# Kernel tuning notes

Measured on AMD Instinct MI355X. Metric: run time of the kernel, lower is better.

Reference implementation:

```python
import jax, jax.numpy as jnp
import numpy as np
import math
from jax import lax

RNN = 256
N_MELS = 80
RF = 5
FRAME = N_MELS * RF  # 400
DYN_CH = 8
DYN_K = 21
STATIC_CH = 8
STATIC_K = 21
PRIOR_LEN = 11


def _betabinom_pmf(n, a, b):
    k = np.arange(n + 1, dtype=np.float64)
    lg = lambda x: np.array([math.lgamma(float(v)) for v in np.atleast_1d(x)])
    logC = lg(n + 1) - lg(k + 1) - lg(n - k + 1)
    logB = lg(k + a) + lg(n - k + b) - lg(np.full_like(k, n + a + b))
    logB0 = math.lgamma(a) + math.lgamma(b) - math.lgamma(a + b)
    return np.exp(logC + logB - logB0)

# prior buffer, flipped as in the torch module (register_buffer('P', ...flip(0)))
PRIOR = jnp.asarray(_betabinom_pmf(PRIOR_LEN - 1, 0.1, 0.9)[::-1].copy(), dtype=jnp.float32)


def gru_cell(x, h, wi, bi, wh, bh):
    # torch GRUCell math
    gi = x @ wi.T + bi
    gh = h @ wh.T + bh
    ir, iz, i_n = jnp.split(gi, 3, axis=-1)
    hr, hz, h_n = jnp.split(gh, 3, axis=-1)
    r = jax.nn.sigmoid(ir + hr)
    z = jax.nn.sigmoid(iz + hz)
    n = jnp.tanh(i_n + r * h_n)
    return (1.0 - z) * n + z * h


def dca(s, alpha, dW_w, dW_b, dV_w, dF_w, dU_w, dT_w, dT_b, dv_w):
    B, S = alpha.shape
    # betabinomial prior: causal conv with flipped pmf
    ap = jnp.pad(alpha, ((0, 0), (PRIOR_LEN - 1, 0)))[:, None, :]  # [B,1,S+10]
    p = lax.conv_general_dilated(ap, PRIOR.reshape(1, 1, -1), (1,), [(0, 0)],
                                 dimension_numbers=('NCH', 'OIH', 'NCH'))[:, 0]  # [B,S]
    p = jnp.log(jnp.clip(p, 1e-6))
    # dynamic filters: one set of 8 kernels per batch element
    G = jnp.tanh(s @ dW_w.T + dW_b) @ dV_w.T  # [B, 8*21]
    g = lax.conv_general_dilated(alpha[None, :, :], G.reshape(B * DYN_CH, 1, DYN_K),
                                 (1,), [((DYN_K - 1) // 2,) * 2],
                                 dimension_numbers=('NCH', 'OIH', 'NCH'),
                                 feature_group_count=B)  # [1, B*8, S]
    g = g.reshape(B, DYN_CH, S).transpose(0, 2, 1)  # [B,S,8]
    # static filters
    f = lax.conv_general_dilated(alpha[:, None, :], dF_w, (1,), [((STATIC_K - 1) // 2,) * 2],
                                 dimension_numbers=('NCH', 'OIH', 'NCH')).transpose(0, 2, 1)  # [B,S,8]
    e = (jnp.tanh(f @ dU_w.T + g @ dT_w.T + dT_b) @ dv_w.T)[..., 0] + p  # [B,S]
    return jax.nn.softmax(e, axis=-1)


def _decode(encoder_outputs, p1_w, p1_b, p2_w, p2_b, a_wi, a_bi, a_wh, a_bh,
            dW_w, dW_b, dV_w, dF_w, dU_w, dT_w, dT_b, dv_w, l_w, l_b,
            g1_wi, g1_bi, g1_wh, g1_bh, g2_wi, g2_bi, g2_wh, g2_bh, pr_w, pr_b, T_dec):
    B, S, _ = encoder_outputs.shape
    frame0 = jnp.zeros((B, FRAME), jnp.float32)
    alpha0 = jnp.zeros((B, S), jnp.float32).at[:, 0].set(1.0)
    ctx0 = jnp.zeros((B, 3 * RNN), jnp.float32)
    h0 = jnp.zeros((B, RNN), jnp.float32)

    def step(carry, _):
        frame, alpha, ctx, h_att, h1, h2 = carry
        # pre-net (eval mode: dropout is identity)
        pre = jax.nn.relu(jax.nn.relu(frame @ p1_w.T + p1_b) @ p2_w.T + p2_b)  # [B,128]
        h_att = gru_cell(jnp.concatenate([ctx, pre], axis=-1), h_att, a_wi, a_bi, a_wh, a_bh)
        alpha = dca(h_att, alpha, dW_w, dW_b, dV_w, dF_w, dU_w, dT_w, dT_b, dv_w)
        ctx = jnp.einsum('bs,bsd->bd', alpha, encoder_outputs)  # [B,768]
        x = jnp.concatenate([ctx, h_att], axis=-1) @ l_w.T + l_b  # [B,256]
        h1 = gru_cell(x, h1, g1_wi, g1_bi, g1_wh, g1_bh)
        x = x + h1
        h2 = gru_cell(x, h2, g2_wi, g2_bi, g2_wh, g2_bh)
        x = x + h2
        out = x @ pr_w.T + pr_b  # [B,400]
        return (out, alpha, ctx, h_att, h1, h2), out

    (_, alphaT, _, _, _, _), outs = lax.scan(step, (frame0, alpha0, ctx0, h0, h0, h0), None, length=T_dec)
    # outs: [T,B,400] -> [B,80,T*5]
    mel = outs.reshape(T_dec, B, N_MELS, RF).transpose(1, 2, 0, 3).reshape(B, N_MELS, T_dec * RF)
    return mel


def setup_inputs() -> dict:
    key = jax.random.key(0)
    ks = iter(jax.random.split(key, 40))
    w = lambda shape: jax.random.normal(next(ks), shape, jnp.float32) * 0.05
    z = lambda shape: jnp.zeros(shape, jnp.float32)
    B, S, D = 64, 512, 768
    return {
        'encoder_outputs': jax.random.normal(next(ks), (B, S, D), jnp.float32),
        'p1_w': w((RNN, FRAME)), 'p1_b': z((RNN,)),
        'p2_w': w((RNN // 2, RNN)), 'p2_b': z((RNN // 2,)),
        'a_wi': w((3 * RNN, 896)), 'a_bi': z((3 * RNN,)), 'a_wh': w((3 * RNN, RNN)), 'a_bh': z((3 * RNN,)),
        'dW_w': w((128, RNN)), 'dW_b': z((128,)),
        'dV_w': w((DYN_CH * DYN_K, 128)),
        'dF_w': w((STATIC_CH, 1, STATIC_K)),
        'dU_w': w((128, STATIC_CH)),
        'dT_w': w((128, DYN_CH)), 'dT_b': z((128,)),
        'dv_w': w((1, 128)),
        'l_w': w((RNN, 4 * RNN)), 'l_b': z((RNN,)),
        'g1_wi': w((3 * RNN, RNN)), 'g1_bi': z((3 * RNN,)), 'g1_wh': w((3 * RNN, RNN)), 'g1_bh': z((3 * RNN,)),
        'g2_wi': w((3 * RNN, RNN)), 'g2_bi': z((3 * RNN,)), 'g2_wh': w((3 * RNN, RNN)), 'g2_bh': z((3 * RNN,)),
        'pr_w': w((FRAME, RNN)), 'pr_b': z((FRAME,)),
        'T_dec': 250,
    }


def reference(encoder_outputs, p1_w, p1_b, p2_w, p2_b, a_wi, a_bi, a_wh, a_bh,
              dW_w, dW_b, dV_w, dF_w, dU_w, dT_w, dT_b, dv_w, l_w, l_b,
              g1_wi, g1_bi, g1_wh, g1_bh, g2_wi, g2_bi, g2_wh, g2_bh, pr_w, pr_b, T_dec):
    return _decode(encoder_outputs, p1_w, p1_b, p2_w, p2_b, a_wi, a_bi, a_wh, a_bh,
                   dW_w, dW_b, dV_w, dF_w, dU_w, dT_w, dT_b, dv_w, l_w, l_b,
                   g1_wi, g1_bi, g1_wh, g1_bh, g2_wi, g2_bi, g2_wh, g2_bh, pr_w, pr_b, T_dec)
```

## Files before the change

### kernel.cpp

```cpp
#include <hip/hip_runtime.h>
#include <cmath>

#define TDEC 250
#define EPS_A 1e-6f

#define NB_GIC  64
#define NB_GA   128
#define NB_WH1  144
#define NB_WH2  152
#define NBLK    160

#define B_CTX(p)  (8192   + (p)*49152)
#define B_HATT(p) (106496 + (p)*16384)
#define B_H1(p)   (139264 + (p)*16384)
#define B_H2(p)   (172032 + (p)*16384)
#define B_GIC(p)  (204800 + (p)*49152)
#define B_GH(p)   (303104 + (p)*49152)
#define B_GH1(p)  (401408 + (p)*49152)
#define B_GH2(p)  (499712 + (p)*49152)
#define ZERO_END  598016
#define CVT_OFF   598016

#define OP1    0u
#define OP2    106496u
#define OAWIP  139264u
#define ODW    237568u
#define ODV    270336u
#define OLW    291840u
#define OG1I   553984u
#define OG2I   750592u
#define OPR    947200u
#define OAWI   1049600u
#define OAWH   1737728u
#define OG1H   1934336u
#define OG2H   2130944u

struct Prior { float v[11]; };

struct KArgs {
  const float *enc;
  const float *p1w,*p1b,*p2w,*p2b;
  const float *awi,*abi,*awh,*abh;
  const float *dWw,*dWb,*dVw,*dFw,*dUw,*dTw,*dTb,*dvw;
  const float *lw,*lb;
  const float *g1wi,*g1bi,*g1wh,*g1bh;
  const float *g2wi,*g2bi,*g2wh,*g2bh;
  const float *prw,*prb;
  float* ws; float* dout;
  Prior pr;
};

__device__ __forceinline__ float gld(const float* p) {
  return __uint_as_float(__hip_atomic_load((const unsigned*)p, __ATOMIC_RELAXED, __HIP_MEMORY_SCOPE_AGENT));
}
__device__ __forceinline__ void gst(float* p, float v) {
  __hip_atomic_store((unsigned*)p, __float_as_uint(v), __ATOMIC_RELAXED, __HIP_MEMORY_SCOPE_AGENT);
}
__device__ __forceinline__ float sigm(float x) { return 1.f / (1.f + expf(-x)); }

__device__ __forceinline__ float dot8(uint4 w, float4 x0, float4 x1) {
  float a;
  a = __uint_as_float(w.x << 16) * x0.x;
  a = fmaf(__uint_as_float(w.x & 0xffff0000u), x0.y, a);
  a = fmaf(__uint_as_float(w.y << 16),         x0.z, a);
  a = fmaf(__uint_as_float(w.y & 0xffff0000u), x0.w, a);
  a = fmaf(__uint_as_float(w.z << 16),         x1.x, a);
  a = fmaf(__uint_as_float(w.z & 0xffff0000u), x1.y, a);
  a = fmaf(__uint_as_float(w.w << 16),         x1.z, a);
  a = fmaf(__uint_as_float(w.w & 0xffff0000u), x1.w, a);
  return a;
}

__global__ __launch_bounds__(256) void k_init(float* ws) {
  int idx = blockIdx.x * 256 + threadIdx.x;
  for (int i = idx; i < ZERO_END; i += gridDim.x * 256) ws[i] = 0.f;
}

struct CvtSeg { const float* src; unsigned dst; unsigned N, K, KP, sstr, soff, mode; };
struct CvtArgs { CvtSeg s[13]; };
__global__ __launch_bounds__(256) void k_cvt(CvtArgs c, unsigned short* wb) {
  for (int seg = 0; seg < 13; ++seg) {
    CvtSeg sg = c.s[seg];
    unsigned short* d = wb + sg.dst;
    unsigned tot = sg.N * sg.KP;
    for (unsigned i = blockIdx.x * 256 + threadIdx.x; i < tot; i += gridDim.x * 256) {
      if (sg.mode == 0) {
        unsigned u = __float_as_uint(sg.src[i]);
        d[i] = (unsigned short)((u + 0x7fffu + ((u >> 16) & 1u)) >> 16);
      } else {
        unsigned n = i / sg.KP, k = i - n * sg.KP;
        unsigned short v = 0;
        if (k < sg.K) {
          unsigned u = __float_as_uint(sg.src[(size_t)n * sg.sstr + sg.soff + k]);
          v = (unsigned short)((u + 0x7fffu + ((u >> 16) & 1u)) >> 16);
        }
        d[(k >> 3) * (sg.N * 8) + n * 8 + (k & 7)] = v;
      }
    }
  }
}

__device__ __forceinline__ void postw(unsigned* fl, int word, unsigned v) {
  asm volatile("s_waitcnt vmcnt(0)" ::: "memory");
  __syncthreads();
  if (threadIdx.x == 0)
    __hip_atomic_store(&fl[blockIdx.x * 32 + word], v, __ATOMIC_RELAXED, __HIP_MEMORY_SCOPE_AGENT);
}
template <int SLP>
__device__ __forceinline__ void pollge(unsigned* fl, int line, int word, unsigned v) {
  while (__hip_atomic_load(&fl[line * 32 + word], __ATOMIC_RELAXED, __HIP_MEMORY_SCOPE_AGENT) < v)
    __builtin_amdgcn_s_sleep(SLP);
}

__global__ __launch_bounds__(1024, 1) void k_decode(KArgs A) {
  __shared__ __align__(16) float sm[16640];
  float* ws = A.ws;
  unsigned* fl = (unsigned*)ws;
  const unsigned short* wb = (const unsigned short*)(ws + CVT_OFF);
  const int blk = blockIdx.x;
  const int tid = threadIdx.x;

  if (blk < 64) {
    const int b = blk, bg = b >> 4;
    float* alpha = sm;
    float* hattl = sm + 512;
    float* h1l   = sm + 768;
    float* h2l   = sm + 1024;
    float* fr    = sm + 1280;
    float* xcat  = sm + 1696;
    float* xl    = sm + 2728;
    float* x2l   = sm + 2984;
    float* x3l   = sm + 3240;
    float* sal   = sm + 3496;
    float* h1s   = sm + 4040;
    float* pre   = sm + 4296;
    float* sgi   = sm + 4424;
    float* sgh   = sm + 5192;
    float* t1    = sm + 5960;
    float* Gl    = sm + 6088;
    float* sdF   = sm + 6264;
    float* sdU   = sm + 6440;
    float* sdT   = sm + 7464;
    float* sdtb  = sm + 8488;
    float* sdv   = sm + 8616;
    float* es    = sm + 8744;
    float* e     = sm + 9768;
    float* red   = sm + 10280;
    int*   wc    = (int*)(sm + 10296);
    float* lv    = sm + 10304;
    short* li    = (short*)(sm + 10816);
    float* pt    = sm + 11072;

    if (tid < 512) alpha[tid] = (tid == 0) ? 1.f : 0.f;
    if (tid < 256) { hattl[tid] = 0.f; h1l[tid] = 0.f; h2l[tid] = 0.f; xcat[768 + tid] = 0.f; }
    if (tid < 416) fr[tid] = 0.f;
    if (tid < 176) sdF[tid] = (tid < 168) ? A.dFw[tid] : 0.f;
    sdU[tid] = A.dUw[tid];
    sdT[tid] = A.dTw[tid];
    if (tid < 128) { sdtb[tid] = A.dTb[tid]; sdv[tid] = A.dvw[tid]; }
    __syncthreads();

    for (int t = 0; t < TDEC; ++t) {
      const int p = t & 1;
      if (tid < 544) { int sg = tid - 10; sal[tid] = (sg >= 0 && sg < 512) ? alpha[sg] : 0.f; }
      __syncthreads();
      {
        int part = tid >> 8, j = tid & 255;
        const float4* xr = (const float4*)fr;
        float a = 0.f;
#pragma unroll
        for (int g = 0; g < 13; ++g) {
          int gg = part * 13 + g;
          uint4 w = *(const uint4*)(wb + OP1 + (size_t)gg * 2048 + j * 8);
          a += dot8(w, xr[gg * 2], xr[gg * 2 + 1]);
        }
        pt[part * 260 + j] = a;
      }
      __syncthreads();
      if (tid < 256) h1s[tid] = fmaxf(pt[tid] + pt[260 + tid] + pt[520 + tid] + pt[780 + tid] + A.p1b[tid], 0.f);
      __syncthreads();
      {
        int part = tid >> 7, j = tid & 127;
        const float4* xr = (const float4*)h1s;
        float a = 0.f;
#pragma unroll
        for (int g = 0; g < 4; ++g) {
          int gg = part * 4 + g;
          uint4 w = *(const uint4*)(wb + OP2 + (size_t)gg * 1024 + j * 8);
          a += dot8(w, xr[gg * 2], xr[gg * 2 + 1]);
        }
        pt[part * 132 + j] = a;
      }
      __syncthreads();
      if (tid < 128) {
        float a = A.p2b[tid];
#pragma unroll
        for (int q = 0; q < 8; ++q) a += pt[q * 132 + tid];
        pre[tid] = fmaxf(a, 0.f);
      }
      __syncthreads();
      float gipre = 0.f;
      if (tid < 768) {
        const float4* xr = (const float4*)pre;
        float a = 0.f;
#pragma unroll
        for (int g = 0; g < 16; ++g) {
          uint4 w = *(const uint4*)(wb + OAWIP + (size_t)g * 6144 + tid * 8);
          a += dot8(w, xr[g * 2], xr[g * 2 + 1]);
        }
        gipre = a;
      } else if (tid < 784) {
        pollge<1>(fl, NB_GIC + bg * 16 + (tid - 768), 0, (unsigned)(t + 1));
      } else if (tid < 788) {
        pollge<1>(fl, NB_GA + bg * 4 + (tid - 784), 0, (unsigned)(t + 1));
      }
      __syncthreads();
      if (tid < 768) {
        sgi[tid] = gipre + gld(ws + B_GIC(p) + b * 768 + tid) + A.abi[tid];
        sgh[tid] = gld(ws + B_GH(p) + b * 768 + tid) + A.abh[tid];
      }
      __syncthreads();
      if (tid < 256) {
        float r = sigm(sgi[tid] + sgh[tid]);
        float z = sigm(sgi[256 + tid] + sgh[256 + tid]);
        float n = tanhf(sgi[512 + tid] + r * sgh[512 + tid]);
        float hnew = (1.f - z) * n + z * hattl[tid];
        hattl[tid] = hnew;
        xcat[768 + tid] = hnew;
        gst(ws + B_HATT(p) + b * 256 + tid, hnew);
      }
      postw(fl, 1, (unsigned)(t + 1));
      {
        int part = tid >> 7, j = tid & 127;
        const float4* xr = (const float4*)hattl;
        float a = 0.f;
#pragma unroll
        for (int g = 0; g < 4; ++g) {
          int gg = part * 4 + g;
          uint4 w = *(const uint4*)(wb + ODW + (size_t)gg * 1024 + j * 8);
          a += dot8(w, xr[gg * 2], xr[gg * 2 + 1]);
        }
        pt[part * 132 + j] = a;
      }
      __syncthreads();
      if (tid < 128) {
        float a = A.dWb[tid];
#pragma unroll
        for (int q = 0; q < 8; ++q) a += pt[q * 132 + tid];
        t1[tid] = tanhf(a);
      }
      __syncthreads();
      if (tid < 672) {
        int part = tid / 168, j = tid - part * 168;
        const float4* xr = (const float4*)t1;
        float a = 0.f;
#pragma unroll
        for (int g = 0; g < 4; ++g) {
          int gg = part * 4 + g;
          uint4 w = *(const uint4*)(wb + ODV + (size_t)gg * 1344 + j * 8);
          a += dot8(w, xr[gg * 2], xr[gg * 2 + 1]);
        }
        pt[part * 172 + j] = a;
      }
      __syncthreads();
      if (tid < 168) Gl[tid] = pt[tid] + pt[172 + tid] + pt[344 + tid] + pt[516 + tid];
      __syncthreads();
      {
        int sl = tid >> 1, half = tid & 1;
        float f0[8], g0[8];
#pragma unroll
        for (int q = 0; q < 8; ++q) {
          float fa = 0.f, ga = 0.f;
#pragma unroll
          for (int k = 0; k < 21; ++k) {
            float a = sal[sl + k];
            fa = fmaf(sdF[q * 21 + k], a, fa);
            ga = fmaf(Gl[q * 21 + k], a, ga);
          }
          f0[q] = fa; g0[q] = ga;
        }
        float acc = 0.f;
        for (int cc = half * 64; cc < half * 64 + 64; ++cc) {
          float a = sdtb[cc];
#pragma unroll
          for (int q = 0; q < 8; ++q)
            a = fmaf(sdU[cc * 8 + q], f0[q], fmaf(sdT[cc * 8 + q], g0[q], a));
          acc = fmaf(sdv[cc], tanhf(a), acc);
        }
        es[sl * 2 + half] = acc;
      }
      __syncthreads();
      if (tid < 512) {
        float pr = 0.f;
#pragma unroll
        for (int k = 0; k < 11; ++k) pr = fmaf(A.pr.v[k], sal[tid + k], pr);
        e[tid] = es[tid * 2] + es[tid * 2 + 1] + logf(fmaxf(pr, 1e-6f));
      }
      __syncthreads();
      {
        int lane = tid & 63, wv = tid >> 6;
        float e0 = (tid < 512) ? e[tid] : -1e30f;
        float m = e0;
        for (int o = 32; o; o >>= 1) m = fmaxf(m, __shfl_xor(m, o));
        if (lane == 0) red[wv] = m;
        __syncthreads();
        m = red[0];
        for (int w = 1; w < 8; ++w) m = fmaxf(m, red[w]);
        float p0 = (tid < 512) ? expf(e0 - m) : 0.f;
        float s = p0;
        for (int o = 32; o; o >>= 1) s += __shfl_xor(s, o);
        __syncthreads();
        if (lane == 0) red[wv] = s;
        __syncthreads();
        float tot = red[0];
        for (int w = 1; w < 8; ++w) tot += red[w];
        float inv = 1.f / tot;
        float a0 = p0 * inv;
        if (tid < 512) alpha[tid] = a0;
        unsigned long long mk = __ballot(tid < 512 && a0 > EPS_A);
        if (lane == 0 && wv < 8) wc[wv] = (int)__popcll(mk);
        __syncthreads();
        int base = 0;
        for (int w = 0; w < wv && w < 8; ++w) base += wc[w];
        int n = 0;
        for (int w = 0; w < 8; ++w) n += wc[w];
        unsigned long long below = (1ull << lane) - 1ull;
        if (tid < 512 && a0 > EPS_A) {
          int pp = base + (int)__popcll(mk & below);
          li[pp] = (short)tid; lv[pp] = a0;
        }
        __syncthreads();
        const float* encb = A.enc + (size_t)b * 512 * 768;
        if (tid < 768) {
          float acc0 = 0.f, acc1 = 0.f;
          int i = 0;
          for (; i + 8 <= n; i += 8) {
            acc0 = fmaf(lv[i],   encb[(size_t)li[i]   * 768 + tid],
                   fmaf(lv[i+1], encb[(size_t)li[i+1] * 768 + tid],
                   fmaf(lv[i+2], encb[(size_t)li[i+2] * 768 + tid],
                   fmaf(lv[i+3], encb[(size_t)li[i+3] * 768 + tid], acc0))));
            acc1 = fmaf(lv[i+4], encb[(size_t)li[i+4] * 768 + tid],
                   fmaf(lv[i+5], encb[(size_t)li[i+5] * 768 + tid],
                   fmaf(lv[i+6], encb[(size_t)li[i+6] * 768 + tid],
                   fmaf(lv[i+7], encb[(size_t)li[i+7] * 768 + tid], acc1))));
          }
          for (; i < n; ++i) acc0 = fmaf(lv[i], encb[(size_t)li[i] * 768 + tid], acc0);
          float acc = acc0 + acc1;
          xcat[tid] = acc;
          gst(ws + B_CTX(p) + b * 768 + tid, acc);
        }
      }
      postw(fl, 0, (unsigned)(t + 1));
      {
        int part = tid >> 8, j = tid & 255;
        const float4* xr = (const float4*)xcat;
        float a = 0.f;
#pragma unroll 16
        for (int g = 0; g < 32; ++g) {
          int gg = part * 32 + g;
          uint4 w = *(const uint4*)(wb + OLW + (size_t)gg * 2048 + j * 8);
          a += dot8(w, xr[gg * 2], xr[gg * 2 + 1]);
        }
        pt[part * 260 + j] = a;
      }
      __syncthreads();
      if (tid < 256) xl[tid] = pt[tid] + pt[260 + tid] + pt[520 + tid] + pt[780 + tid] + A.lb[tid];
      __syncthreads();
      {
        float giv = 0.f;
        if (tid < 768) {
          const float4* xr = (const float4*)xl;
          float a = 0.f;
#pragma unroll 16
          for (int g = 0; g < 32; ++g) {
            uint4 w = *(const uint4*)(wb + OG1I + (size_t)g * 6144 + tid * 8);
            a += dot8(w, xr[g * 2], xr[g * 2 + 1]);
          }
          giv = a;
        } else if (tid < 776) {
          pollge<1>(fl, NB_WH1 + (tid - 768), 0, (unsigned)(t + 1));
        }
        __syncthreads();
        if (tid < 768) {
          sgi[tid] = giv + A.g1bi[tid];
          sgh[tid] = gld(ws + B_GH1(p) + b * 768 + tid);
        }
        __syncthreads();
        if (tid < 256) {
          float r = sigm(sgi[tid] + sgh[tid]);
          float z = sigm(sgi[256 + tid] + sgh[256 + tid]);
          float n = tanhf(sgi[512 + tid] + r * sgh[512 + tid]);
          float hnew = (1.f - z) * n + z * h1l[tid];
          h1l[tid] = hnew;
          gst(ws + B_H1(p) + b * 256 + tid, hnew);
          x2l[tid] = xl[tid] + hnew;
        }
        postw(fl, 2, (unsigned)(t + 1));
      }
      {
        float giv = 0.f;
        if (tid < 768) {
          const float4* xr = (const float4*)x2l;
          float a = 0.f;
#pragma unroll 16
          for (int g = 0; g < 32; ++g) {
            uint4 w = *(const uint4*)(wb + OG2I + (size_t)g * 6144 + tid * 8);
            a += dot8(w, xr[g * 2], xr[g * 2 + 1]);
          }
          giv = a;
        } else if (tid < 776) {
          pollge<1>(fl, NB_WH2 + (tid - 768), 0, (unsigned)(t + 1));
        }
        __syncthreads();
        if (tid < 768) {
          sgi[tid] = giv + A.g2bi[tid];
          sgh[tid] = gld(ws + B_GH2(p) + b * 768 + tid);
        }
        __syncthreads();
        if (tid < 256) {
          float r = sigm(sgi[tid] + sgh[tid]);
          float z = sigm(sgi[256 + tid] + sgh[256 + tid]);
          float n = tanhf(sgi[512 + tid] + r * sgh[512 + tid]);
          float hnew = (1.f - z) * n + z * h2l[tid];
          h2l[tid] = hnew;
          gst(ws + B_H2(p) + b * 256 + tid, hnew);
          x3l[tid] = x2l[tid] + hnew;
        }
        postw(fl, 3, (unsigned)(t + 1));
      }
      if (tid < 800) {
        int part = tid >= 400 ? 1 : 0, j = tid - part * 400;
        const float4* xr = (const float4*)x3l;
        float a = 0.f;
#pragma unroll
        for (int g = 0; g < 16; ++g) {
          int gg = part * 16 + g;
          uint4 w = *(const uint4*)(wb + OPR + (size_t)gg * 3200 + j * 8);
          a += dot8(w, xr[gg * 2], xr[gg * 2 + 1]);
        }
        pt[part * 404 + j] = a;
      }
      __syncthreads();
      if (tid < 400) {
        float v = pt[tid] + pt[404 + tid] + A.prb[tid];
        fr[tid] = v;
        gst(A.dout + (size_t)b * 100000 + (tid / 5) * 1250 + t * 5 + (tid % 5), v);
      }
      __syncthreads();
    }
  } else if (blk < NB_GA) {
    int rb = blk - NB_GIC, bg = rb >> 4, jg = rb & 15;
    int B = bg * 16, R0 = jg * 48;
    float* cl = sm;
    for (int t = 0; t < TDEC; ++t) {
      const int p = t & 1;
      if (tid < 16) pollge<4>(fl, bg * 16 + tid, 0, (unsigned)t);
      __syncthreads();
      for (int idx = tid; idx < 12288; idx += 1024) {
        int bb = idx / 768, k = idx - bb * 768;
        cl[bb * 772 + k] = gld(ws + B_CTX(p ^ 1) + (B + bb) * 768 + k);
      }
      __syncthreads();
      if (tid < 768) {
        int rr = tid >> 4, bb = tid & 15;
        int row = R0 + rr;
        const uint4* wr = (const uint4*)(wb + OAWI + (size_t)row * 896);
        const float4* xr = (const float4*)(cl + bb * 772);
        float a = 0.f;
#pragma unroll 16
        for (int k4 = 0; k4 < 96; ++k4) a += dot8(wr[k4], xr[2*k4], xr[2*k4+1]);
        gst(ws + B_GIC(p) + (B + bb) * 768 + row, a);
      }
      postw(fl, 0, (unsigned)(t + 1));
    }
  } else if (blk < NB_WH1) {
    int rb = blk - NB_GA, bg = rb >> 2, jg = rb & 3;
    int B = bg * 16, R0 = jg * 192;
    float* hl = sm;
    for (int t = 0; t < TDEC; ++t) {
      const int p = t & 1;
      if (tid < 16) pollge<4>(fl, bg * 16 + tid, 1, (unsigned)t);
      __syncthreads();
      for (int idx = tid; idx < 4096; idx += 1024) {
        int bb = idx >> 8, k = idx & 255;
        hl[bb * 260 + k] = gld(ws + B_HATT(p ^ 1) + (B + bb) * 256 + k);
      }
      __syncthreads();
#pragma unroll
      for (int pass = 0; pass < 3; ++pass) {
        int rr = pass * 64 + (tid >> 4), bb = tid & 15;
        int row = R0 + rr;
        const uint4* wr = (const uint4*)(wb + OAWH + (size_t)row * 256);
        const float4* xr = (const float4*)(hl + bb * 260);
        float a = 0.f;
#pragma unroll 16
        for (int k4 = 0; k4 < 32; ++k4) a += dot8(wr[k4], xr[2*k4], xr[2*k4+1]);
        gst(ws + B_GH(p) + (B + bb) * 768 + row, a);
      }
      postw(fl, 0, (unsigned)(t + 1));
    }
  } else {
    const int isW2 = (blk >= NB_WH2);
    const int w = blk - (isW2 ? NB_WH2 : NB_WH1);
    const unsigned OW = isW2 ? OG2H : OG1H;
    const float* bh = isW2 ? A.g2bh : A.g1bh;
    const int hOff0  = isW2 ? B_H2(0)  : B_H1(0);
    const int ghOff0 = isW2 ? B_GH2(0) : B_GH1(0);
    const int word = isW2 ? 3 : 2;
    const int R0 = w * 96;
    float* hl = sm;
    for (int t = 0; t < TDEC; ++t) {
      const int p = t & 1;
      if (tid < 64) pollge<4>(fl, tid, word, (unsigned)t);
      __syncthreads();
      for (int idx = tid; idx < 16384; idx += 1024) {
        int bb = idx >> 8, k = idx & 255;
        hl[bb * 260 + k] = gld(ws + hOff0 + (p ^ 1) * 16384 + bb * 256 + k);
      }
      __syncthreads();
#pragma unroll
      for (int pass = 0; pass < 6; ++pass) {
        int o = pass * 1024 + tid;
        int bb = o & 63, lr = o >> 6;
        int row = R0 + lr;
        const uint4* wr = (const uint4*)(wb + OW + (size_t)row * 256);
        const float4* xr = (const float4*)(hl + bb * 260);
        float a = 0.f;
#pragma unroll 16
        for (int k4 = 0; k4 < 32; ++k4) a += dot8(wr[k4], xr[2*k4], xr[2*k4+1]);
        gst(ws + ghOff0 + p * 49152 + bb * 768 + row, a + bh[row]);
      }
      postw(fl, 0, (unsigned)(t + 1));
    }
  }
}

extern "C" void kernel_launch(void* const* d_in, const int* in_sizes, int n_in,
                              void* d_out, int out_size, void* d_ws, size_t ws_size,
                              hipStream_t stream) {
  (void)in_sizes; (void)n_in; (void)out_size; (void)ws_size;
  KArgs A;
  A.enc  = (const float*)d_in[0];
  A.p1w  = (const float*)d_in[1];  A.p1b  = (const float*)d_in[2];
  A.p2w  = (const float*)d_in[3];  A.p2b  = (const float*)d_in[4];
  A.awi  = (const float*)d_in[5];  A.abi  = (const float*)d_in[6];
  A.awh  = (const float*)d_in[7];  A.abh  = (const float*)d_in[8];
  A.dWw  = (const float*)d_in[9];  A.dWb  = (const float*)d_in[10];
  A.dVw  = (const float*)d_in[11]; A.dFw  = (const float*)d_in[12];
  A.dUw  = (const float*)d_in[13]; A.dTw  = (const float*)d_in[14];
  A.dTb  = (const float*)d_in[15]; A.dvw  = (const float*)d_in[16];
  A.lw   = (const float*)d_in[17]; A.lb   = (const float*)d_in[18];
  A.g1wi = (const float*)d_in[19]; A.g1bi = (const float*)d_in[20];
  A.g1wh = (const float*)d_in[21]; A.g1bh = (const float*)d_in[22];
  A.g2wi = (const float*)d_in[23]; A.g2bi = (const float*)d_in[24];
  A.g2wh = (const float*)d_in[25]; A.g2bh = (const float*)d_in[26];
  A.prw  = (const float*)d_in[27]; A.prb  = (const float*)d_in[28];
  A.ws   = (float*)d_ws;
  A.dout = (float*)d_out;

  {
    double aP = 0.1, bP = 0.9;
    double logB0 = lgamma(aP) + lgamma(bP) - lgamma(aP + bP);
    double pm[11];
    for (int k = 0; k <= 10; ++k) {
      double logC = lgamma(11.0) - lgamma(k + 1.0) - lgamma(11.0 - k);
      double logBt = lgamma(k + aP) + lgamma(10.0 - k + bP) - lgamma(10.0 + aP + bP);
      pm[k] = exp(logC + logBt - logB0);
    }
    for (int k = 0; k < 11; ++k) A.pr.v[k] = (float)pm[10 - k];
  }

  CvtArgs C;
  C.s[0]  = {A.p1w,  OP1,   256, 400, 416, 400, 0, 1};
  C.s[1]  = {A.p2w,  OP2,   128, 256, 256, 256, 0, 1};
  C.s[2]  = {A.awi,  OAWIP, 768, 128, 128, 896, 768, 1};
  C.s[3]  = {A.dWw,  ODW,   128, 256, 256, 256, 0, 1};
  C.s[4]  = {A.dVw,  ODV,   168, 128, 128, 128, 0, 1};
  C.s[5]  = {A.lw,   OLW,   256, 1024, 1024, 1024, 0, 1};
  C.s[6]  = {A.g1wi, OG1I,  768, 256, 256, 256, 0, 1};
  C.s[7]  = {A.g2wi, OG2I,  768, 256, 256, 256, 0, 1};
  C.s[8]  = {A.prw,  OPR,   400, 256, 256, 256, 0, 1};
  C.s[9]  = {A.awi,  OAWI,  768, 896, 896, 896, 0, 0};
  C.s[10] = {A.awh,  OAWH,  768, 256, 256, 256, 0, 0};
  C.s[11] = {A.g1wh, OG1H,  768, 256, 256, 256, 0, 0};
  C.s[12] = {A.g2wh, OG2H,  768, 256, 256, 256, 0, 0};

  k_init<<<256, 256, 0, stream>>>((float*)d_ws);
  k_cvt<<<256, 256, 0, stream>>>(C, (unsigned short*)((float*)d_ws + CVT_OFF));
  k_decode<<<NBLK, 1024, 0, stream>>>(A);
}
```

Before: 29.67 ms.

## Split post-attention decoder stages across partner blocks per batch element

Adds 64 partner blocks, one per batch element. Each partner computes the upper half of the output rows for the linear projection, both GRU input projections and the frame projection, while the main block computes the lower half. Halves are exchanged through workspace buffers and flag polling at each stage. This aims to shorten the serial per-step critical path by halving each block's weight streaming, at the cost of several extra cross-block handshakes per timestep and more blocks that must be co-resident.

```diff
diff --git a/kernel.cpp b/kernel.cpp
--- a/kernel.cpp
+++ b/kernel.cpp
@@ -8,7 +8,8 @@
 #define NB_GA   128
 #define NB_WH1  144
 #define NB_WH2  152
-#define NBLK    160
+#define NB_PART 160
+#define NBLK    224
 
 #define B_CTX(p)  (8192   + (p)*49152)
 #define B_HATT(p) (106496 + (p)*16384)
@@ -18,8 +19,15 @@
 #define B_GH(p)   (303104 + (p)*49152)
 #define B_GH1(p)  (401408 + (p)*49152)
 #define B_GH2(p)  (499712 + (p)*49152)
-#define ZERO_END  598016
-#define CVT_OFF   598016
+#define B_XLO(p)  (598016 + (p)*8192)
+#define B_XH(p)   (614400 + (p)*8192)
+#define B_X2LO(p) (630784 + (p)*8192)
+#define B_X2H(p)  (647168 + (p)*8192)
+#define B_X3LO(p) (663552 + (p)*8192)
+#define B_X3H(p)  (679936 + (p)*8192)
+#define B_FRH(p)  (696320 + (p)*13312)
+#define ZERO_END  722944
+#define CVT_OFF   722944
 
 #define OP1    0u
 #define OP2    106496u
@@ -152,7 +160,8 @@
     float* pt    = sm + 11072;
 
     if (tid < 512) alpha[tid] = (tid == 0) ? 1.f : 0.f;
-    if (tid < 256) { hattl[tid] = 0.f; h1l[tid] = 0.f; h2l[tid] = 0.f; xcat[768 + tid] = 0.f; }
+    if (tid < 256) { hattl[tid] = 0.f; xcat[768 + tid] = 0.f; }
+    if (tid < 128) { h1l[tid] = 0.f; h2l[tid] = 0.f; }
     if (tid < 416) fr[tid] = 0.f;
     if (tid < 176) sdF[tid] = (tid < 168) ? A.dFw[tid] : 0.f;
     sdU[tid] = A.dUw[tid];
@@ -163,6 +172,9 @@
     for (int t = 0; t < TDEC; ++t) {
       const int p = t & 1;
       if (tid < 544) { int sg = tid - 10; sal[tid] = (sg >= 0 && sg < 512) ? alpha[sg] : 0.f; }
+      else if (tid == 544) pollge<1>(fl, NB_PART + b, 3, (unsigned)t);
+      __syncthreads();
+      if (tid >= 200 && tid < 400) fr[tid] = gld(ws + B_FRH(p) + b * 208 + (tid - 200));
       __syncthreads();
       {
         int part = tid >> 8, j = tid & 255;
@@ -352,97 +364,125 @@
       }
       postw(fl, 0, (unsigned)(t + 1));
       {
-        int part = tid >> 8, j = tid & 255;
+        int part = tid >> 7, j = tid & 127;
         const float4* xr = (const float4*)xcat;
         float a = 0.f;
-#pragma unroll 16
-        for (int g = 0; g < 32; ++g) {
-          int gg = part * 32 + g;
+#pragma unroll
+        for (int g = 0; g < 16; ++g) {
+          int gg = part * 16 + g;
           uint4 w = *(const uint4*)(wb + OLW + (size_t)gg * 2048 + j * 8);
           a += dot8(w, xr[gg * 2], xr[gg * 2 + 1]);
         }
-        pt[part * 260 + j] = a;
-      }
-      __syncthreads();
-      if (tid < 256) xl[tid] = pt[tid] + pt[260 + tid] + pt[520 + tid] + pt[780 + tid] + A.lb[tid];
-      __syncthreads();
-      {
-        float giv = 0.f;
+        pt[part * 132 + j] = a;
+      }
+      __syncthreads();
+      if (tid < 128) {
+        float a = A.lb[tid];
+#pragma unroll
+        for (int q = 0; q < 8; ++q) a += pt[q * 132 + tid];
+        xl[tid] = a;
+        gst(ws + B_XLO(p) + b * 128 + tid, a);
+      }
+      postw(fl, 4, (unsigned)(t + 1));
+      if (tid == 0) pollge<1>(fl, NB_PART + b, 0, (unsigned)(t + 1));
+      __syncthreads();
+      if (tid < 128) xl[128 + tid] = gld(ws + B_XH(p) + b * 128 + tid);
+      __syncthreads();
+      {
         if (tid < 768) {
+          int part = tid >= 384, ri = tid - part * 384;
+          int row = ((ri >> 7) << 8) + (ri & 127);
           const float4* xr = (const float4*)xl;
           float a = 0.f;
-#pragma unroll 16
-          for (int g = 0; g < 32; ++g) {
-            uint4 w = *(const uint4*)(wb + OG1I + (size_t)g * 6144 + tid * 8);
-            a += dot8(w, xr[g * 2], xr[g * 2 + 1]);
+#pragma unroll
+          for (int g = 0; g < 16; ++g) {
+            int gg = part * 16 + g;
+            uint4 w = *(const uint4*)(wb + OG1I + (size_t)gg * 6144 + row * 8);
+            a += dot8(w, xr[gg * 2], xr[gg * 2 + 1]);
           }
-          giv = a;
+          pt[part * 384 + ri] = a;
         } else if (tid < 776) {
           pollge<1>(fl, NB_WH1 + (tid - 768), 0, (unsigned)(t + 1));
         }
         __syncthreads();
-        if (tid < 768) {
-          sgi[tid] = giv + A.g1bi[tid];
-          sgh[tid] = gld(ws + B_GH1(p) + b * 768 + tid);
-        }
-        __syncthreads();
-        if (tid < 256) {
+        if (tid < 384) {
+          int row = ((tid >> 7) << 8) + (tid & 127);
+          sgi[tid] = pt[tid] + pt[384 + tid] + A.g1bi[row];
+          sgh[tid] = gld(ws + B_GH1(p) + b * 768 + row);
+        }
+        __syncthreads();
+        if (tid < 128) {
           float r = sigm(sgi[tid] + sgh[tid]);
-          float z = sigm(sgi[256 + tid] + sgh[256 + tid]);
-          float n = tanhf(sgi[512 + tid] + r * sgh[512 + tid]);
+          float z = sigm(sgi[128 + tid] + sgh[128 + tid]);
+          float n = tanhf(sgi[256 + tid] + r * sgh[256 + tid]);
           float hnew = (1.f - z) * n + z * h1l[tid];
           h1l[tid] = hnew;
           gst(ws + B_H1(p) + b * 256 + tid, hnew);
-          x2l[tid] = xl[tid] + hnew;
+          float x2v = xl[tid] + hnew;
+          x2l[tid] = x2v;
+          gst(ws + B_X2LO(p) + b * 128 + tid, x2v);
         }
         postw(fl, 2, (unsigned)(t + 1));
-      }
-      {
-        float giv = 0.f;
+        if (tid == 0) pollge<1>(fl, NB_PART + b, 1, (unsigned)(t + 1));
+        __syncthreads();
+        if (tid < 128) x2l[128 + tid] = gld(ws + B_X2H(p) + b * 128 + tid);
+        __syncthreads();
+      }
+      {
         if (tid < 768) {
+          int part = tid >= 384, ri = tid - part * 384;
+          int row = ((ri >> 7) << 8) + (ri & 127);
           const float4* xr = (const float4*)x2l;
           float a = 0.f;
-#pragma unroll 16
-          for (int g = 0; g < 32; ++g) {
-            uint4 w = *(const uint4*)(wb + OG2I + (size_t)g * 6144 + tid * 8);
-            a += dot8(w, xr[g * 2], xr[g * 2 + 1]);
+#pragma unroll
+          for (int g = 0; g < 16; ++g) {
+            int gg = part * 16 + g;
+            uint4 w = *(const uint4*)(wb + OG2I + (size_t)gg * 6144 + row * 8);
+            a += dot8(w, xr[gg * 2], xr[gg * 2 + 1]);
           }
-          giv = a;
+          pt[part * 384 + ri] = a;
         } else if (tid < 776) {
           pollge<1>(fl, NB_WH2 + (tid - 768), 0, (unsigned)(t + 1));
         }
         __syncthreads();
-        if (tid < 768) {
-          sgi[tid] = giv + A.g2bi[tid];
-          sgh[tid] = gld(ws + B_GH2(p) + b * 768 + tid);
-        }
-        __syncthreads();
-        if (tid < 256) {
+        if (tid < 384) {
+          int row = ((tid >> 7) << 8) + (tid & 127);
+          sgi[tid] = pt[tid] + pt[384 + tid] + A.g2bi[row];
+          sgh[tid] = gld(ws + B_GH2(p) + b * 768 + row);
+        }
+        __syncthreads();
+        if (tid < 128) {
           float r = sigm(sgi[tid] + sgh[tid]);
-          float z = sigm(sgi[256 + tid] + sgh[256 + tid]);
-          float n = tanhf(sgi[512 + tid] + r * sgh[512 + tid]);
+          float z = sigm(sgi[128 + tid] + sgh[128 + tid]);
+          float n = tanhf(sgi[256 + tid] + r * sgh[256 + tid]);
           float hnew = (1.f - z) * n + z * h2l[tid];
           h2l[tid] = hnew;
           gst(ws + B_H2(p) + b * 256 + tid, hnew);
-          x3l[tid] = x2l[tid] + hnew;
+          float x3v = x2l[tid] + hnew;
+          x3l[tid] = x3v;
+          gst(ws + B_X3LO(p) + b * 128 + tid, x3v);
         }
         postw(fl, 3, (unsigned)(t + 1));
+        if (tid == 0) pollge<1>(fl, NB_PART + b, 2, (unsigned)(t + 1));
+        __syncthreads();
+        if (tid < 128) x3l[128 + tid] = gld(ws + B_X3H(p) + b * 128 + tid);
+        __syncthreads();
       }
       if (tid < 800) {
-        int part = tid >= 400 ? 1 : 0, j = tid - part * 400;
+        int part = tid / 200, j = tid - part * 200;
         const float4* xr = (const float4*)x3l;
         float a = 0.f;
 #pragma unroll
-        for (int g = 0; g < 16; ++g) {
-          int gg = part * 16 + g;
+        for (int g = 0; g < 8; ++g) {
+          int gg = part * 8 + g;
           uint4 w = *(const uint4*)(wb + OPR + (size_t)gg * 3200 + j * 8);
           a += dot8(w, xr[gg * 2], xr[gg * 2 + 1]);
         }
-        pt[part * 404 + j] = a;
-      }
-      __syncthreads();
-      if (tid < 400) {
-        float v = pt[tid] + pt[404 + tid] + A.prb[tid];
+        pt[part * 204 + j] = a;
+      }
+      __syncthreads();
+      if (tid < 200) {
+        float v = pt[tid] + pt[204 + tid] + pt[408 + tid] + pt[612 + tid] + A.prb[tid];
         fr[tid] = v;
         gst(A.dout + (size_t)b * 100000 + (tid / 5) * 1250 + t * 5 + (tid % 5), v);
       }
@@ -499,7 +539,7 @@
       }
       postw(fl, 0, (unsigned)(t + 1));
     }
-  } else {
+  } else if (blk < NB_PART) {
     const int isW2 = (blk >= NB_WH2);
     const int w = blk - (isW2 ? NB_WH2 : NB_WH1);
     const unsigned OW = isW2 ? OG2H : OG1H;
@@ -507,11 +547,15 @@
     const int hOff0  = isW2 ? B_H2(0)  : B_H1(0);
     const int ghOff0 = isW2 ? B_GH2(0) : B_GH1(0);
     const int word = isW2 ? 3 : 2;
+    const int pword = isW2 ? 2 : 1;
     const int R0 = w * 96;
     float* hl = sm;
     for (int t = 0; t < TDEC; ++t) {
       const int p = t & 1;
-      if (tid < 64) pollge<4>(fl, tid, word, (unsigned)t);
+      if (tid < 64) {
+        pollge<4>(fl, tid, word, (unsigned)t);
+        pollge<4>(fl, NB_PART + tid, pword, (unsigned)t);
+      }
       __syncthreads();
       for (int idx = tid; idx < 16384; idx += 1024) {
         int bb = idx >> 8, k = idx & 255;
@@ -531,6 +575,153 @@
         gst(ws + ghOff0 + p * 49152 + bb * 768 + row, a + bh[row]);
       }
       postw(fl, 0, (unsigned)(t + 1));
+    }
+  } else {
+    const int b = blk - NB_PART;
+    float* xcat = sm;
+    float* xl   = sm + 1032;
+    float* x2l  = sm + 1288;
+    float* x3l  = sm + 1544;
+    float* h1h  = sm + 1800;
+    float* h2h  = sm + 1928;
+    float* sgiP = sm + 2056;
+    float* sghP = sm + 2440;
+    float* pt   = sm + 2824;
+    if (tid < 128) { h1h[tid] = 0.f; h2h[tid] = 0.f; }
+    __syncthreads();
+    for (int t = 0; t < TDEC; ++t) {
+      const int p = t & 1;
+      if (tid == 0) pollge<1>(fl, b, 0, (unsigned)(t + 1));
+      else if (tid == 1) pollge<1>(fl, b, 1, (unsigned)(t + 1));
+      __syncthreads();
+      if (tid < 768) xcat[tid] = gld(ws + B_CTX(p) + b * 768 + tid);
+      else xcat[tid] = gld(ws + B_HATT(p) + b * 256 + (tid - 768));
+      __syncthreads();
+      {
+        int part = tid >> 7, j = tid & 127;
+        const float4* xr = (const float4*)xcat;
+        float a = 0.f;
+#pragma unroll
+        for (int g = 0; g < 16; ++g) {
+          int gg = part * 16 + g;
+          uint4 w = *(const uint4*)(wb + OLW + (size_t)gg * 2048 + (128 + j) * 8);
+          a += dot8(w, xr[gg * 2], xr[gg * 2 + 1]);
+        }
+        pt[part * 132 + j] = a;
+      }
+      __syncthreads();
+      if (tid < 128) {
+        float a = A.lb[128 + tid];
+#pragma unroll
+        for (int q = 0; q < 8; ++q) a += pt[q * 132 + tid];
+        xl[128 + tid] = a;
+        gst(ws + B_XH(p) + b * 128 + tid, a);
+      }
+      postw(fl, 0, (unsigned)(t + 1));
+      if (tid == 0) pollge<1>(fl, b, 4, (unsigned)(t + 1));
+      __syncthreads();
+      if (tid < 128) xl[tid] = gld(ws + B_XLO(p) + b * 128 + tid);
+      __syncthreads();
+      {
+        if (tid < 768) {
+          int part = tid >= 384, ri = tid - part * 384;
+          int row = ((ri >> 7) << 8) + 128 + (ri & 127);
+          const float4* xr = (const float4*)xl;
+          float a = 0.f;
+#pragma unroll
+          for (int g = 0; g < 16; ++g) {
+            int gg = part * 16 + g;
+            uint4 w = *(const uint4*)(wb + OG1I + (size_t)gg * 6144 + row * 8);
+            a += dot8(w, xr[gg * 2], xr[gg * 2 + 1]);
+          }
+          pt[part * 384 + ri] = a;
+        } else if (tid < 776) {
+          pollge<1>(fl, NB_WH1 + (tid - 768), 0, (unsigned)(t + 1));
+        }
+        __syncthreads();
+        if (tid < 384) {
+          int row = ((tid >> 7) << 8) + 128 + (tid & 127);
+          sgiP[tid] = pt[tid] + pt[384 + tid] + A.g1bi[row];
+          sghP[tid] = gld(ws + B_GH1(p) + b * 768 + row);
+        }
+        __syncthreads();
+        if (tid < 128) {
+          float r = sigm(sgiP[tid] + sghP[tid]);
+          float z = sigm(sgiP[128 + tid] + sghP[128 + tid]);
+          float n = tanhf(sgiP[256 + tid] + r * sghP[256 + tid]);
+          float hnew = (1.f - z) * n + z * h1h[tid];
+          h1h[tid] = hnew;
+          gst(ws + B_H1(p) + b * 256 + 128 + tid, hnew);
+          float x2v = xl[128 + tid] + hnew;
+          x2l[128 + tid] = x2v;
+          gst(ws + B_X2H(p) + b * 128 + tid, x2v);
+        }
+        postw(fl, 1, (unsigned)(t + 1));
+        if (tid == 0) pollge<1>(fl, b, 2, (unsigned)(t + 1));
+        __syncthreads();
+        if (tid < 128) x2l[tid] = gld(ws + B_X2LO(p) + b * 128 + tid);
+        __syncthreads();
+      }
+      {
+        if (tid < 768) {
+          int part = tid >= 384, ri = tid - part * 384;
+          int row = ((ri >> 7) << 8) + 128 + (ri & 127);
+          const float4* xr = (const float4*)x2l;
+          float a = 0.f;
+#pragma unroll
+          for (int g = 0; g < 16; ++g) {
+            int gg = part * 16 + g;
+            uint4 w = *(const uint4*)(wb + OG2I + (size_t)gg * 6144 + row * 8);
+            a += dot8(w, xr[gg * 2], xr[gg * 2 + 1]);
+          }
+          pt[part * 384 + ri] = a;
+        } else if (tid < 776) {
+          pollge<1>(fl, NB_WH2 + (tid - 768), 0, (unsigned)(t + 1));
+        }
+        __syncthreads();
+        if (tid < 384) {
+          int row = ((tid >> 7) << 8) + 128 + (tid & 127);
+          sgiP[tid] = pt[tid] + pt[384 + tid] + A.g2bi[row];
+          sghP[tid] = gld(ws + B_GH2(p) + b * 768 + row);
+        }
+        __syncthreads();
+        if (tid < 128) {
+          float r = sigm(sgiP[tid] + sghP[tid]);
+          float z = sigm(sgiP[128 + tid] + sghP[128 + tid]);
+          float n = tanhf(sgiP[256 + tid] + r * sghP[256 + tid]);
+          float hnew = (1.f - z) * n + z * h2h[tid];
+          h2h[tid] = hnew;
+          gst(ws + B_H2(p) + b * 256 + 128 + tid, hnew);
+          float x3v = x2l[128 + tid] + hnew;
+          x3l[128 + tid] = x3v;
+          gst(ws + B_X3H(p) + b * 128 + tid, x3v);
+        }
+        postw(fl, 2, (unsigned)(t + 1));
+        if (tid == 0) pollge<1>(fl, b, 3, (unsigned)(t + 1));
+        __syncthreads();
+        if (tid < 128) x3l[tid] = gld(ws + B_X3LO(p) + b * 128 + tid);
+        __syncthreads();
+      }
+      if (tid < 800) {
+        int part = tid / 200, j = tid - part * 200;
+        const float4* xr = (const float4*)x3l;
+        float a = 0.f;
+#pragma unroll
+        for (int g = 0; g < 8; ++g) {
+          int gg = part * 8 + g;
+          uint4 w = *(const uint4*)(wb + OPR + (size_t)gg * 3200 + (200 + j) * 8);
+          a += dot8(w, xr[gg * 2], xr[gg * 2 + 1]);
+        }
+        pt[part * 204 + j] = a;
+      }
+      __syncthreads();
+      if (tid < 200) {
+        int row = 200 + tid;
+        float v = pt[tid] + pt[204 + tid] + pt[408 + tid] + pt[612 + tid] + A.prb[row];
+        gst(ws + B_FRH((t + 1) & 1) + b * 208 + tid, v);
+        gst(A.dout + (size_t)b * 100000 + (row / 5) * 1250 + t * 5 + (row % 5), v);
+      }
+      postw(fl, 3, (unsigned)(t + 1));
     }
   }
 }
```

Measured after the change: 31.66 ms. 6.7% more time.
